# Kernel tuning notes

Hardware: AMD Instinct MI355X
Metric: run time of the kernel (lower is better)

## Reference

```python
import jax, jax.numpy as jnp
import numpy as np

D_MODEL = 1024


def setup_inputs() -> dict:
    key = jax.random.key(0)
    ks = jax.random.split(key, 8)
    B, S, D = 32, 2048, D_MODEL
    scale = 1.0 / np.sqrt(D)
    return {
        "query": jax.random.normal(ks[0], (B, D), dtype=jnp.float32),
        "keys": jax.random.normal(ks[1], (B, S, D), dtype=jnp.float32),
        "Wq_w": jax.random.normal(ks[2], (D, D), dtype=jnp.float32) * scale,
        "Wq_b": jax.random.normal(ks[3], (D,), dtype=jnp.float32) * 0.01,
        "Wk_w": jax.random.normal(ks[4], (D, D), dtype=jnp.float32) * scale,
        "Wk_b": jax.random.normal(ks[5], (D,), dtype=jnp.float32) * 0.01,
        "v_w": jax.random.normal(ks[6], (D,), dtype=jnp.float32) * scale,
        "v_b": jax.random.normal(ks[7], (1,), dtype=jnp.float32) * 0.01,
    }


def reference(query, keys, Wq_w, Wq_b, Wk_w, Wk_b, v_w, v_b):
    # q: [B, 1, D], k: [B, S, D]
    q = (query @ Wq_w.T + Wq_b)[:, None, :]
    k = keys @ Wk_w.T + Wk_b
    # additive (Bahdanau) scores: [B, S]
    scores = jnp.einsum("bsd,d->bs", jnp.tanh(q + k), v_w) + v_b[0]
    attn = jax.nn.softmax(scores, axis=-1)
    # weighted sum over original keys: [B, D]
    context = jnp.einsum("bs,bsd->bd", attn, keys)
    return (context, attn)
```

## Files before the change

### kernel.cpp

```cpp
#include <hip/hip_runtime.h>
#include <cstddef>
#include <cstdint>

#define BATCH 32
#define SEQ 2048
#define DM 1024

typedef __attribute__((ext_vector_type(8))) _Float16 half8v;
typedef __attribute__((ext_vector_type(4))) _Float16 half4v;
typedef __attribute__((ext_vector_type(4))) float f32x4;

__device__ _Float16 g_Bpk[8 * 8 * 32 * 4 * 16 * 8];
__device__ float g_q[BATCH * DM];
__device__ float g_sp[16][BATCH * SEQ];

__device__ __forceinline__ float tanh_fast(float x) {
    float e = __expf(2.0f * x);
    return 1.0f - 2.0f / (e + 1.0f);
}

__global__ __launch_bounds__(256) void packb_kernel(const float* __restrict__ Wk_w) {
    int blk = blockIdx.x;
    int nc = blk >> 3, sub = blk & 7;
    int t = threadIdx.x;
    int row = t & 15, kgrp = (t >> 4) & 3, kt0 = t >> 6;
    const float* src = Wk_w + (size_t)(nc * 128 + sub * 16 + row) * DM;
    _Float16* dst = g_Bpk + (size_t)blk * 16384;
#pragma unroll
    for (int pass = 0; pass < 8; ++pass) {
        int kt = pass * 4 + kt0;
        float4 w0 = *reinterpret_cast<const float4*>(src + kt * 32 + kgrp * 8);
        float4 w1 = *reinterpret_cast<const float4*>(src + kt * 32 + kgrp * 8 + 4);
        union { _Float16 f[8]; half8v v; } h;
        h.f[0] = (_Float16)w0.x; h.f[1] = (_Float16)w0.y;
        h.f[2] = (_Float16)w0.z; h.f[3] = (_Float16)w0.w;
        h.f[4] = (_Float16)w1.x; h.f[5] = (_Float16)w1.y;
        h.f[6] = (_Float16)w1.z; h.f[7] = (_Float16)w1.w;
        *reinterpret_cast<half8v*>(&dst[(size_t)((kt * 4 + kgrp) * 16 + row) * 8]) = h.v;
    }
}

__global__ __launch_bounds__(256) void init_kernel(float* __restrict__ context) {
    int idx = blockIdx.x * 256 + threadIdx.x;
    if (idx < BATCH * DM) context[idx] = 0.f;
}

__global__ __launch_bounds__(256) void qproj_kernel(const float* __restrict__ query,
                                                    const float* __restrict__ Wq_w,
                                                    const float* __restrict__ Wq_b) {
    int d = blockIdx.x;
    int t = threadIdx.x;
    __shared__ float wrow[DM];
    __shared__ float part[8][32];
    reinterpret_cast<float4*>(wrow)[t] =
        reinterpret_cast<const float4*>(Wq_w + (size_t)d * DM)[t];
    __syncthreads();
    int b = t & 31, seg = t >> 5;
    const float4* qp = reinterpret_cast<const float4*>(query + b * DM + seg * 128);
    const float4* wp = reinterpret_cast<const float4*>(wrow + seg * 128);
    float acc = 0.f;
#pragma unroll
    for (int i = 0; i < 32; ++i) {
        float4 qv = qp[i];
        float4 wv = wp[i];
        acc += qv.x * wv.x + qv.y * wv.y + qv.z * wv.z + qv.w * wv.w;
    }
    part[seg][b] = acc;
    __syncthreads();
    if (t < 32) {
        float s = Wq_b[d];
#pragma unroll
        for (int g = 0; g < 8; ++g) s += part[g][t];
        g_q[t * DM + d] = s;
    }
}

#define BM 128
#define BN 128
#define BK 32
#define NT (DM / BK)

__global__ __launch_bounds__(256, 3) void scores_kernel(const float* __restrict__ keys,
                                                        const float* __restrict__ Wk_b,
                                                        const float* __restrict__ v_w) {
    __shared__ _Float16 AhS[2][4][BM + 1][8];

    const unsigned bid = blockIdx.x;
    const unsigned L = (bid & 7u) * 512u + (bid >> 3);
    const int mtile = (int)(L >> 3);
    const int nchunk = (int)(L & 7u);
    const int m0 = mtile * BM;
    const int n0 = nchunk * BN;
    const int b = m0 >> 11;

    const int t = threadIdx.x;
    const int w = t >> 6, l = t & 63;
    const int wm = w >> 1, wn = w & 1;
    const int lr = l & 15, lg = l >> 4;

    const int akc = (l & 7) >> 1;
    const int aoff = ((l & 7) & 1) * 4;
    const float* Ap = keys + (size_t)(m0 + w * 32 + (l >> 3)) * DM + (l & 7) * 4;

    const _Float16* Bp = g_Bpk + ((size_t)(nchunk * 8 + wn * 4)) * 16384
                               + (size_t)(l >> 4) * 128 + (size_t)(l & 15) * 8;

    float4 as[4];
    half8v bE[4], bO[4];

    f32x4 acc[4][4];
#pragma unroll
    for (int mi = 0; mi < 4; ++mi)
#pragma unroll
        for (int ni = 0; ni < 4; ++ni)
#pragma unroll
            for (int c = 0; c < 4; ++c) acc[mi][ni][c] = 0.f;

#define LOAD_A(kt)                                                               \
    {                                                                            \
        _Pragma("unroll") for (int j = 0; j < 4; ++j)                            \
            as[j] = *reinterpret_cast<const float4*>(                            \
                Ap + (size_t)j * 8 * DM + (kt) * BK);                            \
    }
#define LOAD_BF(kt, dst)                                                         \
    {                                                                            \
        _Pragma("unroll") for (int ni = 0; ni < 4; ++ni)                         \
            dst[ni] = *reinterpret_cast<const half8v*>(                          \
                Bp + (size_t)ni * 16384 + (size_t)(kt) * 512);                   \
    }
#define STAGE_A(bufi)                                                            \
    {                                                                            \
        _Pragma("unroll") for (int j = 0; j < 4; ++j) {                          \
            const float* fa = reinterpret_cast<const float*>(&as[j]);            \
            union { _Float16 f[4]; half4v v; } h;                                \
            h.f[0] = (_Float16)fa[0]; h.f[1] = (_Float16)fa[1];                  \
            h.f[2] = (_Float16)fa[2]; h.f[3] = (_Float16)fa[3];                  \
            *reinterpret_cast<half4v*>(                                          \
                &AhS[bufi][akc][w * 32 + j * 8 + (l >> 3)][aoff]) = h.v;         \
        }                                                                        \
    }
#define COMPUTE(bufi, breg)                                                      \
    {                                                                            \
        __builtin_amdgcn_s_setprio(1);                                           \
        _Pragma("unroll") for (int mi = 0; mi < 4; ++mi) {                       \
            half8v ahv = *reinterpret_cast<const half8v*>(                       \
                &AhS[bufi][lg][wm * 64 + mi * 16 + lr][0]);                      \
            _Pragma("unroll") for (int ni = 0; ni < 4; ++ni)                     \
                acc[mi][ni] = __builtin_amdgcn_mfma_f32_16x16x32_f16(            \
                    ahv, breg[ni], acc[mi][ni], 0, 0, 0);                        \
        }                                                                        \
        __builtin_amdgcn_s_setprio(0);                                          \
    }

    LOAD_A(0);
    STAGE_A(0);
    LOAD_A(1);
    LOAD_BF(0, bE);
    __syncthreads();

    for (int tt = 0; tt + 1 < NT; tt += 2) {
        LOAD_BF(tt + 1, bO);
        COMPUTE(0, bE);
        STAGE_A(1);
        if (tt + 2 < NT) LOAD_A(tt + 2);
        __syncthreads();

        if (tt + 2 < NT) LOAD_BF(tt + 2, bE);
        COMPUTE(1, bO);
        if (tt + 2 < NT) STAGE_A(0);
        if (tt + 3 < NT) LOAD_A(tt + 3);
        __syncthreads();
    }

    float qb[4], vw[4];
#pragma unroll
    for (int ni = 0; ni < 4; ++ni) {
        int n = n0 + wn * 64 + ni * 16 + lr;
        qb[ni] = g_q[b * DM + n] + Wk_b[n];
        vw[ni] = v_w[n];
    }
#pragma unroll
    for (int mi = 0; mi < 4; ++mi) {
#pragma unroll
        for (int rg = 0; rg < 4; ++rg) {
            float p = 0.f;
#pragma unroll
            for (int ni = 0; ni < 4; ++ni) {
                float val = acc[mi][ni][rg] + qb[ni];
                p += tanh_fast(val) * vw[ni];
            }
#pragma unroll
            for (int off = 8; off >= 1; off >>= 1) p += __shfl_xor(p, off, 16);
            if (lr == 0)
                g_sp[nchunk * 2 + wn][m0 + wm * 64 + mi * 16 + lg * 4 + rg] = p;
        }
    }
#undef LOAD_A
#undef LOAD_BF
#undef STAGE_A
#undef COMPUTE
}

__global__ __launch_bounds__(256) void softmax_kernel(float* __restrict__ attn) {
    int b = blockIdx.x;
    int tid = threadIdx.x;
    __shared__ float redm[4];
    __shared__ float reds[4];
    float v[8];
    float mx = -1e30f;
#pragma unroll
    for (int i = 0; i < 8; ++i) {
        int idx = b * SEQ + i * 256 + tid;
        float s = 0.f;
#pragma unroll
        for (int pslot = 0; pslot < 16; ++pslot) s += g_sp[pslot][idx];
        v[i] = s;
        mx = fmaxf(mx, v[i]);
    }
#pragma unroll
    for (int off = 32; off >= 1; off >>= 1) mx = fmaxf(mx, __shfl_xor(mx, off));
    int wid = tid >> 6;
    if ((tid & 63) == 0) redm[wid] = mx;
    __syncthreads();
    mx = fmaxf(fmaxf(redm[0], redm[1]), fmaxf(redm[2], redm[3]));
    float sum = 0.f;
#pragma unroll
    for (int i = 0; i < 8; ++i) {
        v[i] = expf(v[i] - mx);
        sum += v[i];
    }
#pragma unroll
    for (int off = 32; off >= 1; off >>= 1) sum += __shfl_xor(sum, off);
    if ((tid & 63) == 0) reds[wid] = sum;
    __syncthreads();
    sum = reds[0] + reds[1] + reds[2] + reds[3];
    float inv = 1.f / sum;
#pragma unroll
    for (int i = 0; i < 8; ++i) attn[b * SEQ + i * 256 + tid] = v[i] * inv;
}

__global__ __launch_bounds__(256) void context_kernel(const float* __restrict__ keys,
                                                      const float* __restrict__ attn,
                                                      float* __restrict__ context) {
    int id = blockIdx.x;
    int schunk = id & 15;
    int b = id >> 4;
    int tid = threadIdx.x;
    __shared__ float a_s[128];
    if (tid < 128) a_s[tid] = attn[b * SEQ + schunk * 128 + tid];
    __syncthreads();
    const float4* kp =
        reinterpret_cast<const float4*>(keys + ((size_t)b * SEQ + schunk * 128) * DM) + tid;
    float4 acc = {0.f, 0.f, 0.f, 0.f};
#pragma unroll 4
    for (int s = 0; s < 128; ++s) {
        float4 kv = kp[(size_t)s * (DM / 4)];
        float a = a_s[s];
        acc.x += a * kv.x; acc.y += a * kv.y; acc.z += a * kv.z; acc.w += a * kv.w;
    }
    atomicAdd(&context[b * DM + tid * 4 + 0], acc.x);
    atomicAdd(&context[b * DM + tid * 4 + 1], acc.y);
    atomicAdd(&context[b * DM + tid * 4 + 2], acc.z);
    atomicAdd(&context[b * DM + tid * 4 + 3], acc.w);
}

extern "C" void kernel_launch(void* const* d_in, const int* in_sizes, int n_in,
                              void* d_out, int out_size, void* d_ws, size_t ws_size,
                              hipStream_t stream) {
    const float* query = (const float*)d_in[0];
    const float* keys  = (const float*)d_in[1];
    const float* Wq_w  = (const float*)d_in[2];
    const float* Wq_b  = (const float*)d_in[3];
    const float* Wk_w  = (const float*)d_in[4];
    const float* Wk_b  = (const float*)d_in[5];
    const float* v_w   = (const float*)d_in[6];

    float* context = (float*)d_out;
    float* attn    = context + BATCH * DM;

    hipLaunchKernelGGL(packb_kernel, dim3(64), dim3(256), 0, stream, Wk_w);
    hipLaunchKernelGGL(init_kernel, dim3(128), dim3(256), 0, stream, context);
    hipLaunchKernelGGL(qproj_kernel, dim3(DM), dim3(256), 0, stream, query, Wq_w, Wq_b);
    hipLaunchKernelGGL(scores_kernel, dim3((BATCH * SEQ / BM) * (DM / BN)), dim3(256), 0, stream,
                       keys, Wk_b, v_w);
    hipLaunchKernelGGL(softmax_kernel, dim3(BATCH), dim3(256), 0, stream, attn);
    hipLaunchKernelGGL(context_kernel, dim3(512), dim3(256), 0, stream, keys, attn, context);
}
```

Measured before the change: 271.7 us.

## Double-buffer A global loads in registers, issue earlier, use packed fp16 convert

The A-tile register staging gets two register sets, so the global load for step tt+2 is issued before the MFMA compute of step tt instead of after it. This hides more global-memory latency. The fp32-to-fp16 conversion now uses packed cvt_pkrtz, which rounds toward zero instead of to nearest. __syncthreads is replaced by an explicit lgkmcnt wait plus s_barrier, so the barrier no longer waits for outstanding global loads. The cost is higher register pressure and a small change in rounding precision.

```diff
diff --git a/kernel.cpp b/kernel.cpp
--- a/kernel.cpp
+++ b/kernel.cpp
@@ -8,6 +8,7 @@
 
 typedef __attribute__((ext_vector_type(8))) _Float16 half8v;
 typedef __attribute__((ext_vector_type(4))) _Float16 half4v;
+typedef __attribute__((ext_vector_type(2))) __fp16 fp16x2;
 typedef __attribute__((ext_vector_type(4))) float f32x4;
 
 __device__ _Float16 g_Bpk[8 * 8 * 32 * 4 * 16 * 8];
@@ -105,7 +106,7 @@
     const _Float16* Bp = g_Bpk + ((size_t)(nchunk * 8 + wn * 4)) * 16384
                                + (size_t)(l >> 4) * 128 + (size_t)(l & 15) * 8;
 
-    float4 as[4];
+    float4 asE[4], asO[4];
     half8v bE[4], bO[4];
 
     f32x4 acc[4][4];
@@ -116,10 +117,10 @@
 #pragma unroll
             for (int c = 0; c < 4; ++c) acc[mi][ni][c] = 0.f;
 
-#define LOAD_A(kt)                                                               \
+#define LOAD_A(kt, dst)                                                          \
     {                                                                            \
         _Pragma("unroll") for (int j = 0; j < 4; ++j)                            \
-            as[j] = *reinterpret_cast<const float4*>(                            \
+            dst[j] = *reinterpret_cast<const float4*>(                           \
                 Ap + (size_t)j * 8 * DM + (kt) * BK);                            \
     }
 #define LOAD_BF(kt, dst)                                                         \
@@ -128,15 +129,15 @@
             dst[ni] = *reinterpret_cast<const half8v*>(                          \
                 Bp + (size_t)ni * 16384 + (size_t)(kt) * 512);                   \
     }
-#define STAGE_A(bufi)                                                            \
+#define STAGE_A(bufi, areg)                                                      \
     {                                                                            \
         _Pragma("unroll") for (int j = 0; j < 4; ++j) {                          \
-            const float* fa = reinterpret_cast<const float*>(&as[j]);            \
-            union { _Float16 f[4]; half4v v; } h;                                \
-            h.f[0] = (_Float16)fa[0]; h.f[1] = (_Float16)fa[1];                  \
-            h.f[2] = (_Float16)fa[2]; h.f[3] = (_Float16)fa[3];                  \
+            const float* fa = reinterpret_cast<const float*>(&areg[j]);          \
+            union { fp16x2 h2[2]; half4v v; } u;                                 \
+            u.h2[0] = __builtin_amdgcn_cvt_pkrtz(fa[0], fa[1]);                  \
+            u.h2[1] = __builtin_amdgcn_cvt_pkrtz(fa[2], fa[3]);                  \
             *reinterpret_cast<half4v*>(                                          \
-                &AhS[bufi][akc][w * 32 + j * 8 + (l >> 3)][aoff]) = h.v;         \
+                &AhS[bufi][akc][w * 32 + j * 8 + (l >> 3)][aoff]) = u.v;         \
         }                                                                        \
     }
 #define COMPUTE(bufi, breg)                                                      \
@@ -151,25 +152,29 @@
         }                                                                        \
         __builtin_amdgcn_s_setprio(0);                                          \
     }
-
-    LOAD_A(0);
-    STAGE_A(0);
-    LOAD_A(1);
+#define SYNC()                                                                   \
+    asm volatile("s_waitcnt lgkmcnt(0)" ::: "memory");                           \
+    __builtin_amdgcn_s_barrier();                                                \
+    asm volatile("" ::: "memory");
+
+    LOAD_A(0, asE);
     LOAD_BF(0, bE);
-    __syncthreads();
-
-    for (int tt = 0; tt + 1 < NT; tt += 2) {
+    STAGE_A(0, asE);
+    LOAD_A(1, asO);
+    SYNC()
+
+    for (int tt = 0; tt < NT; tt += 2) {
         LOAD_BF(tt + 1, bO);
+        if (tt + 2 < NT) LOAD_A(tt + 2, asE);
         COMPUTE(0, bE);
-        STAGE_A(1);
-        if (tt + 2 < NT) LOAD_A(tt + 2);
-        __syncthreads();
+        STAGE_A(1, asO);
+        SYNC()
 
         if (tt + 2 < NT) LOAD_BF(tt + 2, bE);
+        if (tt + 3 < NT) LOAD_A(tt + 3, asO);
         COMPUTE(1, bO);
-        if (tt + 2 < NT) STAGE_A(0);
-        if (tt + 3 < NT) LOAD_A(tt + 3);
-        __syncthreads();
+        if (tt + 2 < NT) STAGE_A(0, asE);
+        SYNC()
     }
 
     float qb[4], vw[4];
@@ -199,6 +204,7 @@
 #undef LOAD_BF
 #undef STAGE_A
 #undef COMPUTE
+#undef SYNC
 }
 
 __global__ __launch_bounds__(256) void softmax_kernel(float* __restrict__ attn) {
```

Result: no change. 270.1 us (-0.6%).
